# Kernel tuning notes

Hardware: AMD Instinct MI355X
Metric: run time of the kernel (lower is better)

The kernel has to match this reference:

```python
import jax, jax.numpy as jnp
import numpy as np

B, S, D = 8, 512, 512
H, DK = 64, 8          # 64 heads hardcoded in SelfAttentiveLBLBiLM
WIDTH = 16             # local window width
NL = 2                 # highway layers
N = S + 2 * WIDTH      # padded sequence length


def setup_inputs() -> dict:
    key = jax.random.key(0)
    ks = jax.random.split(key, 12)
    s = 0.02
    return {
        "inputs": jax.random.normal(ks[0], (B, S, D), jnp.float32),
        "left_pad": jax.random.normal(ks[1], (WIDTH, D), jnp.float32) * s,
        "right_pad": jax.random.normal(ks[2], (WIDTH, D), jnp.float32) * s,
        "l_Wqkv": jax.random.normal(ks[3], (3, D, D), jnp.float32) * s,
        "l_bqkv": jnp.zeros((3, D), jnp.float32),
        "l_Wo": jax.random.normal(ks[4], (D, D), jnp.float32) * s,
        "l_bo": jnp.zeros((D,), jnp.float32),
        "r_Wqkv": jax.random.normal(ks[5], (3, D, D), jnp.float32) * s,
        "r_bqkv": jnp.zeros((3, D), jnp.float32),
        "r_Wo": jax.random.normal(ks[6], (D, D), jnp.float32) * s,
        "r_bo": jnp.zeros((D,), jnp.float32),
        "lhw_W": jax.random.normal(ks[7], (NL, 2 * D, D), jnp.float32) * s,
        "lhw_b": jnp.zeros((NL, 2 * D), jnp.float32),
        "rhw_W": jax.random.normal(ks[8], (NL, 2 * D, D), jnp.float32) * s,
        "rhw_b": jnp.zeros((NL, 2 * D), jnp.float32),
    }


def _masks(n, width):
    i = jnp.arange(n)[:, None]
    j = jnp.arange(n)[None, :]
    # local_mask: triu(k=-width-1) * (1 - triu(k=1)) -> i-width-1 <= j <= i
    left = (j <= i) & (j >= i - width - 1)
    # right mask is the full flip of the left mask
    right = (j >= i) & (j <= i + width + 1)
    return left, right


def _mha(x, Wqkv, bqkv, Wo, bo, mask):
    b, n, d = x.shape
    # torch Linear: y = x @ W.T + b, W is [out, in]
    qkv = jnp.einsum("bnd,tod->tbno", x, Wqkv) + bqkv[:, None, None, :]
    q, k, v = [t.reshape(b, n, H, DK).transpose(0, 2, 1, 3) for t in qkv]
    scores = jnp.einsum("bhqd,bhkd->bhqk", q, k) / jnp.sqrt(jnp.float32(DK))
    scores = jnp.where(mask[None, None], scores, jnp.float32(-1e9))
    p = jax.nn.softmax(scores, axis=-1)
    out = jnp.einsum("bhqk,bhkd->bhqd", p, v)
    out = out.transpose(0, 2, 1, 3).reshape(b, n, d)
    return out @ Wo.T + bo


def _highway(x, Ws, bs):
    for l in range(NL):
        proj = x @ Ws[l].T + bs[l]
        nonlin = jax.nn.relu(proj[..., :D])
        gate = jax.nn.sigmoid(proj[..., D:])
        x = gate * x + (1.0 - gate) * nonlin
    return x


def reference(inputs, left_pad, right_pad, l_Wqkv, l_bqkv, l_Wo, l_bo,
              r_Wqkv, r_bqkv, r_Wo, r_bo, lhw_W, lhw_b, rhw_W, rhw_b):
    b = inputs.shape[0]
    new_inputs = jnp.concatenate(
        [jnp.broadcast_to(left_pad[None], (b, WIDTH, D)), inputs,
         jnp.broadcast_to(right_pad[None], (b, WIDTH, D))], axis=1)  # [B, N, D]
    left_mask, right_mask = _masks(N, WIDTH)
    new_left = _mha(new_inputs, l_Wqkv, l_bqkv, l_Wo, l_bo, left_mask)
    new_right = _mha(new_inputs, r_Wqkv, r_bqkv, r_Wo, r_bo, right_mask)
    # per-step loop indexes position start + width -> slice [WIDTH : WIDTH + S]
    left_out = _highway(new_left[:, WIDTH:WIDTH + S], lhw_W, lhw_b)
    right_out = _highway(new_right[:, WIDTH:WIDTH + S], rhw_W, rhw_b)
    last = jnp.concatenate([left_out, right_out], axis=-1)  # [B, S, 2D]
    all_layers = last[None]  # [1, B, S, 2D] (single layer stacked on dim 0)
    return (all_layers, last)
```

## Files before the change

### kernel.cpp

```cpp
#include <hip/hip_runtime.h>
#include <math.h>

#define B_ 8
#define S_ 512
#define D_ 512
#define WIDTH_ 16
#define NSEQ 544
#define MROWS 4352
#define MOUT 4096
#define OUTHALF 4194304

typedef _Float16 half8 __attribute__((ext_vector_type(8)));
typedef _Float16 half4 __attribute__((ext_vector_type(4)));
typedef float floatx4 __attribute__((ext_vector_type(4)));

#define GLD16(g, l) __builtin_amdgcn_global_load_lds(                          \
    (const __attribute__((address_space(1))) void*)(g),                        \
    (__attribute__((address_space(3))) void*)(l), 16, 0, 0)

#define WAIT_VM(n)  asm volatile("s_waitcnt vmcnt(" #n ")" ::: "memory")
#define WAIT_LGKM0() asm volatile("s_waitcnt lgkmcnt(0)" ::: "memory")
#define BARRIER()                                                              \
    do {                                                                       \
        __builtin_amdgcn_s_barrier();                                          \
        asm volatile("" ::: "memory");                                         \
    } while (0)

__device__ __forceinline__ float sigmoidf_(float x) {
    return 1.f / (1.f + __expf(-x));
}

__device__ __forceinline__ void xcd_swz(const int nx, const int ny,
                                        int& bx, int& by, int& bz) {
    const int flat = blockIdx.x + nx * (blockIdx.y + ny * blockIdx.z);
    const int nwg  = nx * ny * 2;
    const int t2   = (flat & 7) * (nwg >> 3) + (flat >> 3);
    bz = t2 / (nx * ny);
    const int rem = t2 - bz * nx * ny;
    by = rem / nx;
    bx = rem - by * nx;
}

__global__ __launch_bounds__(256)
void gemm_qkv(const _Float16* __restrict__ A,
              const _Float16* __restrict__ B0, const _Float16* __restrict__ B1,
              const float* __restrict__ bias0, const float* __restrict__ bias1,
              _Float16* __restrict__ C16) {
    const int lda = 512, ldb = 512, ldc = 1536;
    __shared__ _Float16 SH[16384];
    int bx, by, bz;
    xcd_swz(12, 34, bx, by, bz);
    const int t    = threadIdx.x;
    const int wave = t >> 6;
    const int lane = t & 63;
    const int bm = by * 128;
    const int bn = bx * 128;
    const int z  = bz;
    const _Float16* B = z ? B1 : B0;
    const float* bias = z ? bias1 : bias0;
    _Float16* C = C16 + (size_t)z * MROWS * 1536;
    const int wm = (wave & 1) * 64;
    const int wn = (wave >> 1) * 64;

    const int inst = wave * 2;
    const int r0 = inst * 16 + (lane >> 2);
    const int kf = (lane & 3) * 8;

    const _Float16* Ag0 = A + (size_t)(bm + r0) * lda + kf;
    const _Float16* Ag1 = Ag0 + (size_t)16 * lda;
    const _Float16* Bg0 = B + (size_t)(bn + r0) * ldb + kf;
    const _Float16* Bg1 = Bg0 + (size_t)16 * ldb;
    const int so = inst * 512;

    const int fr = lane & 15;
    const int fq = (lane >> 4) * 8;

    floatx4 acc[4][4] = {};

#define QKV_STAGE(bf_, koff_)                                                  \
    do {                                                                       \
        GLD16(Ag0 + (koff_), &SH[(bf_) * 4096 + so]);                          \
        GLD16(Ag1 + (koff_), &SH[(bf_) * 4096 + so + 512]);                    \
        GLD16(Bg0 + (koff_), &SH[8192 + (bf_) * 4096 + so]);                   \
        GLD16(Bg1 + (koff_), &SH[8192 + (bf_) * 4096 + so + 512]);             \
    } while (0)

    QKV_STAGE(0, 0);
    QKV_STAGE(1, 32);

#pragma unroll
    for (int tt = 0; tt < 16; tt++) {
        const int c = tt & 1;
        if (tt == 15) WAIT_VM(0);
        else          WAIT_VM(4);
        BARRIER();
        half8 af[4], bf[4];
#pragma unroll
        for (int s = 0; s < 4; s++) {
            af[s] = *(const half8*)&SH[c * 4096 + (wm + s * 16 + fr) * 32 + fq];
            bf[s] = *(const half8*)&SH[8192 + c * 4096 + (wn + s * 16 + fr) * 32 + fq];
        }
        WAIT_LGKM0();
        BARRIER();
        if (tt + 2 < 16) QKV_STAGE(c, (tt + 2) * 32);
#pragma unroll
        for (int i = 0; i < 4; i++)
#pragma unroll
            for (int j = 0; j < 4; j++)
                acc[i][j] = __builtin_amdgcn_mfma_f32_16x16x32_f16(
                    af[i], bf[j], acc[i][j], 0, 0, 0);
    }
#undef QKV_STAGE

    const int rq = (lane >> 4) * 4;
    const int cc = lane & 15;
#pragma unroll
    for (int i = 0; i < 4; i++) {
#pragma unroll
        for (int j = 0; j < 4; j++) {
            const int col = wn + j * 16 + cc;
            const float bv = bias[bn + col];
#pragma unroll
            for (int r = 0; r < 4; r++)
                SH[(wm + i * 16 + rq + r) * 128 + col] =
                    (_Float16)(acc[i][j][r] + bv);
        }
    }
    WAIT_LGKM0();
    BARRIER();
#pragma unroll
    for (int it = 0; it < 8; it++) {
        const int flat = it * 256 + t;
        const int row = flat >> 4;
        const int ch  = flat & 15;
        *(half8*)&C[(size_t)(bm + row) * ldc + bn + ch * 8] =
            *(const half8*)&SH[row * 128 + ch * 8];
    }
}

__global__ __launch_bounds__(256)
void gemm_wo(const _Float16* __restrict__ Aall,
             const _Float16* __restrict__ B0, const _Float16* __restrict__ B1,
             const float* __restrict__ bias0, const float* __restrict__ bias1,
             _Float16* __restrict__ x16base) {
    const int lda = 512, ldb = 512;
    __shared__ _Float16 As[2][64 * 32];
    __shared__ _Float16 Bs[2][128 * 32];
    int bx, by, bz;
    xcd_swz(4, 68, bx, by, bz);
    const int t    = threadIdx.x;
    const int wave = t >> 6;
    const int lane = t & 63;
    const int bm = by * 64;
    const int bn = bx * 128;
    const int z  = bz;
    const _Float16* A = Aall + (size_t)z * MROWS * 512;
    const _Float16* B = z ? B1 : B0;
    const float* bias = z ? bias1 : bias0;
    _Float16* x16 = x16base + (size_t)z * MOUT * 512;

    const int wm = (wave & 1) * 32;
    const int wn = (wave >> 1) * 64;

    const int rA = wave * 16 + (lane >> 2);
    const int rB = wave * 32 + (lane >> 2);
    const int kf = (lane & 3) * 8;

    const _Float16* Ag0 = A + (size_t)(bm + rA) * lda + kf;
    const _Float16* Bg0 = B + (size_t)(bn + rB) * ldb + kf;
    const _Float16* Bg1 = Bg0 + (size_t)16 * ldb;
    const int soA = wave * 512;
    const int soB = wave * 1024;

    const int fr = lane & 15;
    const int fq = (lane >> 4) * 8;

    floatx4 acc[2][4] = {};

#define WO_STAGE(bf_, koff_)                                                   \
    do {                                                                       \
        GLD16(Ag0 + (koff_), &As[bf_][soA]);                                   \
        GLD16(Bg0 + (koff_), &Bs[bf_][soB]);                                   \
        GLD16(Bg1 + (koff_), &Bs[bf_][soB + 512]);                             \
    } while (0)

    WO_STAGE(0, 0);
    WO_STAGE(1, 32);

#pragma unroll
    for (int tt = 0; tt < 16; tt++) {
        const int c = tt & 1;
        if (tt == 15) WAIT_VM(0);
        else          WAIT_VM(3);
        BARRIER();
        half8 af[2], bf[4];
#pragma unroll
        for (int s = 0; s < 2; s++)
            af[s] = *(const half8*)&As[c][(wm + s * 16 + fr) * 32 + fq];
#pragma unroll
        for (int s = 0; s < 4; s++)
            bf[s] = *(const half8*)&Bs[c][(wn + s * 16 + fr) * 32 + fq];
        WAIT_LGKM0();
        BARRIER();
        if (tt + 2 < 16) WO_STAGE(c, (tt + 2) * 32);
#pragma unroll
        for (int i = 0; i < 2; i++)
#pragma unroll
            for (int j = 0; j < 4; j++)
                acc[i][j] = __builtin_amdgcn_mfma_f32_16x16x32_f16(
                    af[i], bf[j], acc[i][j], 0, 0, 0);
    }
#undef WO_STAGE

    const int rq = (lane >> 4) * 4;
    const int cc = lane & 15;
#pragma unroll
    for (int i = 0; i < 2; i++) {
        const int rbase = bm + wm + i * 16 + rq;
#pragma unroll
        for (int r = 0; r < 4; r++) {
            const int row = rbase + r;
            const int b = row / NSEQ;
            const int s = row - b * NSEQ;
            if (s < WIDTH_ || s >= WIDTH_ + S_) continue;
            const int m = b * S_ + s - WIDTH_;
#pragma unroll
            for (int j = 0; j < 4; j++) {
                const int col = bn + wn + j * 16 + cc;
                x16[(size_t)m * 512 + col] = (_Float16)(acc[i][j][r] + bias[col]);
            }
        }
    }
}

__global__ __launch_bounds__(256)
void gemm_hw(const _Float16* __restrict__ x16inbase,
             const _Float16* __restrict__ W0, const _Float16* __restrict__ W1,
             const float* __restrict__ b0, const float* __restrict__ b1,
             _Float16* __restrict__ x16outbase,
             float* __restrict__ outlastbase,
             float* __restrict__ outallbase) {
    const int lda = 512, ldb = 512;
    __shared__ _Float16 SA[8192];
    __shared__ _Float16 Bn[2][64 * 32];
    __shared__ _Float16 Bg[2][64 * 32];
    int bx, by, bz;
    xcd_swz(8, 32, bx, by, bz);
    const int t    = threadIdx.x;
    const int wave = t >> 6;
    const int lane = t & 63;
    const int bm = by * 128;
    const int bn = bx * 64;
    const int z  = bz;
    const _Float16* A = x16inbase + (size_t)z * MOUT * 512;
    const _Float16* W = z ? W1 : W0;
    const float* bias = z ? b1 : b0;
    _Float16* x16out = x16outbase ? x16outbase + (size_t)z * MOUT * 512 : nullptr;

    const int wm = (wave & 1) * 64;
    const int wn = (wave >> 1) * 32;

    const int rA = wave * 32 + (lane >> 2);
    const int rB = wave * 16 + (lane >> 2);
    const int kf = (lane & 3) * 8;

    const _Float16* Ag0 = A + (size_t)(bm + rA) * lda + kf;
    const _Float16* Ag1 = Ag0 + (size_t)16 * lda;
    const _Float16* Bn0 = W + (size_t)(bn + rB) * ldb + kf;
    const _Float16* Bg0 = W + (size_t)(512 + bn + rB) * ldb + kf;
    const int soA = wave * 1024;
    const int soB = wave * 512;

    const int fr = lane & 15;
    const int fq = (lane >> 4) * 8;

    floatx4 accn[4][2] = {};
    floatx4 accg[4][2] = {};

#define HW_STAGE(bf_, koff_)                                                   \
    do {                                                                       \
        GLD16(Ag0 + (koff_), &SA[(bf_) * 4096 + soA]);                         \
        GLD16(Ag1 + (koff_), &SA[(bf_) * 4096 + soA + 512]);                   \
        GLD16(Bn0 + (koff_), &Bn[bf_][soB]);                                   \
        GLD16(Bg0 + (koff_), &Bg[bf_][soB]);                                   \
    } while (0)

    HW_STAGE(0, 0);
    HW_STAGE(1, 32);

#pragma unroll
    for (int tt = 0; tt < 16; tt++) {
        const int c = tt & 1;
        if (tt == 15) WAIT_VM(0);
        else          WAIT_VM(4);
        BARRIER();
        half8 af[4], bnf[2], bgf[2];
#pragma unroll
        for (int s = 0; s < 4; s++)
            af[s] = *(const half8*)&SA[c * 4096 + (wm + s * 16 + fr) * 32 + fq];
#pragma unroll
        for (int s = 0; s < 2; s++) {
            bnf[s] = *(const half8*)&Bn[c][(wn + s * 16 + fr) * 32 + fq];
            bgf[s] = *(const half8*)&Bg[c][(wn + s * 16 + fr) * 32 + fq];
        }
        WAIT_LGKM0();
        BARRIER();
        if (tt + 2 < 16) HW_STAGE(c, (tt + 2) * 32);
#pragma unroll
        for (int i = 0; i < 4; i++)
#pragma unroll
            for (int j = 0; j < 2; j++) {
                accn[i][j] = __builtin_amdgcn_mfma_f32_16x16x32_f16(
                    af[i], bnf[j], accn[i][j], 0, 0, 0);
                accg[i][j] = __builtin_amdgcn_mfma_f32_16x16x32_f16(
                    af[i], bgf[j], accg[i][j], 0, 0, 0);
            }
    }
#undef HW_STAGE

    const int rq = (lane >> 4) * 4;
    const int cc = lane & 15;
    if (x16out) {
#pragma unroll
        for (int i = 0; i < 4; i++) {
#pragma unroll
            for (int j = 0; j < 2; j++) {
                const int col = wn + j * 16 + cc;
                const float bnl = bias[bn + col];
                const float bgt = bias[512 + bn + col];
#pragma unroll
                for (int r = 0; r < 4; r++) {
                    const int row = wm + i * 16 + rq + r;
                    const float nl = fmaxf(accn[i][j][r] + bnl, 0.f);
                    const float g  = sigmoidf_(accg[i][j][r] + bgt);
                    const float xo = (float)A[(size_t)(bm + row) * 512 + bn + col];
                    SA[row * 64 + col] = (_Float16)(g * xo + (1.f - g) * nl);
                }
            }
        }
        WAIT_LGKM0();
        BARRIER();
#pragma unroll
        for (int it = 0; it < 4; it++) {
            const int flat = it * 256 + t;
            const int row = flat >> 3;
            const int ch  = flat & 7;
            *(half8*)&x16out[(size_t)(bm + row) * 512 + bn + ch * 8] =
                *(const half8*)&SA[row * 64 + ch * 8];
        }
    } else {
        float* outlast = outlastbase + z * 512;
        float* outall  = outallbase  + z * 512;
#pragma unroll
        for (int i = 0; i < 4; i++) {
            const int rbase = bm + wm + i * 16 + rq;
#pragma unroll
            for (int j = 0; j < 2; j++) {
                const int col = bn + wn + j * 16 + cc;
                const float bnl = bias[col];
                const float bgt = bias[512 + col];
#pragma unroll
                for (int r = 0; r < 4; r++) {
                    const int row = rbase + r;
                    const float nl = fmaxf(accn[i][j][r] + bnl, 0.f);
                    const float g  = sigmoidf_(accg[i][j][r] + bgt);
                    const float xo = (float)A[(size_t)row * 512 + col];
                    const float v  = g * xo + (1.f - g) * nl;
                    outlast[(size_t)row * 1024 + col] = v;
                    outall[(size_t)row * 1024 + col] = v;
                }
            }
        }
    }
}

__global__ __launch_bounds__(256)
void attn_win(const _Float16* __restrict__ qkvall, _Float16* __restrict__ attall) {
    const int sb  = (blockIdx.x & 7) * 68 + (blockIdx.x >> 3);
    const int wid = threadIdx.x >> 6;
    const int h   = threadIdx.x & 63;
    const int wflat = sb * 4 + wid;
    const int ig  = wflat % 136;
    const int db  = wflat / 136;
    const int b   = db & 7;
    const int dir = db >> 3;
    const int i0  = ig * 4;
    const int dlo = dir ? 0 : -17;
    const _Float16* qkv = qkvall + (size_t)dir * MROWS * 1536;
    _Float16* att = attall + (size_t)dir * MROWS * 512;
    const size_t rowb = (size_t)b * NSEQ;
    const float scale = 0.35355339059327373f;

    float q[4][8];
#pragma unroll
    for (int tq = 0; tq < 4; tq++) {
        const half8 q8 = *(const half8*)(qkv + (rowb + i0 + tq) * 1536 + h * 8);
#pragma unroll
        for (int d = 0; d < 8; d++) q[tq][d] = (float)q8[d];
    }

    float o[4][8] = {};
    float sum[4] = {};
    const int j0 = i0 + dlo;

#pragma unroll
    for (int jj = 0; jj < 21; jj++) {
        const int j = j0 + jj;
        if (j < 0 || j > NSEQ - 1) continue;
        const size_t jbase = (rowb + j) * 1536 + h * 8;
        const half8 k8 = *(const half8*)(qkv + jbase + 512);
        const half8 v8 = *(const half8*)(qkv + jbase + 1024);
        float kv[8], vv[8];
#pragma unroll
        for (int d = 0; d < 8; d++) { kv[d] = (float)k8[d]; vv[d] = (float)v8[d]; }
#pragma unroll
        for (int tq = 0; tq < 4; tq++) {
            if (jj < tq || jj > tq + 17) continue;
            float d = 0.f;
#pragma unroll
            for (int dd = 0; dd < 8; dd++) d = fmaf(q[tq][dd], kv[dd], d);
            const float p = __expf(d * scale);
            sum[tq] += p;
#pragma unroll
            for (int dd = 0; dd < 8; dd++) o[tq][dd] = fmaf(p, vv[dd], o[tq][dd]);
        }
    }

#pragma unroll
    for (int tq = 0; tq < 4; tq++) {
        const float inv = 1.f / sum[tq];
        half8 o16;
#pragma unroll
        for (int d = 0; d < 8; d++) o16[d] = (_Float16)(o[tq][d] * inv);
        *(half8*)&att[(rowb + i0 + tq) * 512 + h * 8] = o16;
    }
}

__global__ void prep(const float* __restrict__ lq, const float* __restrict__ rq,
                     const float* __restrict__ lo, const float* __restrict__ ro,
                     const float* __restrict__ lh, const float* __restrict__ rh,
                     _Float16* __restrict__ wdst,
                     const float* __restrict__ inp,
                     const float* __restrict__ lp,
                     const float* __restrict__ rp,
                     _Float16* __restrict__ padX) {
    const int gb = blockIdx.x;
    if (gb < 4096) {
        int idx = gb * 256 + threadIdx.x;
        const float* src; int off;
        if      (idx < 196608) { src = lq; off = idx; }
        else if (idx < 393216) { src = rq; off = idx - 196608; }
        else if (idx < 458752) { src = lo; off = idx - 393216; }
        else if (idx < 524288) { src = ro; off = idx - 458752; }
        else if (idx < 786432) { src = lh; off = idx - 524288; }
        else                   { src = rh; off = idx - 786432; }
        const float4 v = ((const float4*)src)[off];
        half4 h = { (_Float16)v.x, (_Float16)v.y, (_Float16)v.z, (_Float16)v.w };
        ((half4*)wdst)[idx] = h;
    } else {
        int idx = (gb - 4096) * 256 + threadIdx.x;
        const int c4 = idx & 127;
        const int t  = idx >> 7;
        const int n = t % NSEQ;
        const int b = t / NSEQ;
        const float* src;
        if (n < WIDTH_)            src = lp + n * 512;
        else if (n < WIDTH_ + S_)  src = inp + ((size_t)(b * S_ + n - WIDTH_)) * 512;
        else                       src = rp + (n - WIDTH_ - S_) * 512;
        const float4 v = *(const float4*)(src + c4 * 4);
        half4 h = { (_Float16)v.x, (_Float16)v.y, (_Float16)v.z, (_Float16)v.w };
        *(half4*)&padX[(size_t)t * 512 + c4 * 4] = h;
    }
}

extern "C" void kernel_launch(void* const* d_in, const int* in_sizes, int n_in,
                              void* d_out, int out_size, void* d_ws, size_t ws_size,
                              hipStream_t stream) {
    const float* inputs    = (const float*)d_in[0];
    const float* left_pad  = (const float*)d_in[1];
    const float* right_pad = (const float*)d_in[2];
    const float* l_Wqkv = (const float*)d_in[3];
    const float* l_bqkv = (const float*)d_in[4];
    const float* l_Wo   = (const float*)d_in[5];
    const float* l_bo   = (const float*)d_in[6];
    const float* r_Wqkv = (const float*)d_in[7];
    const float* r_bqkv = (const float*)d_in[8];
    const float* r_Wo   = (const float*)d_in[9];
    const float* r_bo   = (const float*)d_in[10];
    const float* lhw_W  = (const float*)d_in[11];
    const float* lhw_b  = (const float*)d_in[12];
    const float* rhw_W  = (const float*)d_in[13];
    const float* rhw_b  = (const float*)d_in[14];

    float* out = (float*)d_out;
    _Float16* h = (_Float16*)d_ws;

    _Float16* padX16 = h;
    _Float16* w16    = h + 2228224;
    _Float16* lqkv16 = w16;
    _Float16* rqkv16 = w16 + 786432;
    _Float16* lWo16  = w16 + 1572864;
    _Float16* rWo16  = w16 + 1835008;
    _Float16* lhw16  = w16 + 2097152;
    _Float16* rhw16  = w16 + 3145728;
    _Float16* qkv16  = h + 6422528;
    _Float16* att16  = h + 19791872;
    _Float16* x16a   = h + 24248320;
    _Float16* x16b   = h + 28442624;

    float* out_all  = out;
    float* out_last = out + OUTHALF;

    prep<<<6272, 256, 0, stream>>>(l_Wqkv, r_Wqkv, l_Wo, r_Wo, lhw_W, rhw_W, w16,
                                   inputs, left_pad, right_pad, padX16);

    gemm_qkv<<<dim3(12, 34, 2), 256, 0, stream>>>(
        padX16, lqkv16, rqkv16, l_bqkv, r_bqkv, qkv16);

    attn_win<<<dim3(544), 256, 0, stream>>>(qkv16, att16);

    gemm_wo<<<dim3(4, 68, 2), 256, 0, stream>>>(
        att16, lWo16, rWo16, l_bo, r_bo, x16a);

    gemm_hw<<<dim3(8, 32, 2), 256, 0, stream>>>(
        x16a, lhw16, rhw16, lhw_b, rhw_b, x16b, nullptr, nullptr);
    gemm_hw<<<dim3(8, 32, 2), 256, 0, stream>>>(
        x16b, lhw16 + 524288, rhw16 + 524288, lhw_b + 1024, rhw_b + 1024,
        nullptr, out_last, out_all);
}
```

Baseline: 185.4 us.

## Triple-buffer GEMM K-loops and stage epilogues through LDS for coalesced stores

Moves the three GEMM kernels (qkv, wo, highway) from double to triple LDS buffering. The prefetch for stage tt+2 is now issued right after the first barrier, which removes the second barrier in each K iteration. The wo and highway epilogues now stage results in shared memory and write them back as vectorized, coalesced stores. The highway kernel also bulk-loads its residual input tile into LDS instead of doing scattered global reads. The cost is more LDS per block, which could reduce occupancy, plus extra barriers in the epilogues.

```diff
diff --git a/kernel.cpp b/kernel.cpp
--- a/kernel.cpp
+++ b/kernel.cpp
@@ -19,7 +19,11 @@
     (__attribute__((address_space(3))) void*)(l), 16, 0, 0)
 
 #define WAIT_VM(n)  asm volatile("s_waitcnt vmcnt(" #n ")" ::: "memory")
-#define WAIT_LGKM0() asm volatile("s_waitcnt lgkmcnt(0)" ::: "memory")
+#define WAIT_LGKM0()                                                           \
+    do {                                                                       \
+        asm volatile("s_waitcnt lgkmcnt(0)" ::: "memory");                     \
+        __builtin_amdgcn_sched_barrier(0);                                     \
+    } while (0)
 #define BARRIER()                                                              \
     do {                                                                       \
         __builtin_amdgcn_s_barrier();                                          \
@@ -47,7 +51,7 @@
               const float* __restrict__ bias0, const float* __restrict__ bias1,
               _Float16* __restrict__ C16) {
     const int lda = 512, ldb = 512, ldc = 1536;
-    __shared__ _Float16 SH[16384];
+    __shared__ _Float16 SH[24576];
     int bx, by, bz;
     xcd_swz(12, 34, bx, by, bz);
     const int t    = threadIdx.x;
@@ -81,8 +85,8 @@
     do {                                                                       \
         GLD16(Ag0 + (koff_), &SH[(bf_) * 4096 + so]);                          \
         GLD16(Ag1 + (koff_), &SH[(bf_) * 4096 + so + 512]);                    \
-        GLD16(Bg0 + (koff_), &SH[8192 + (bf_) * 4096 + so]);                   \
-        GLD16(Bg1 + (koff_), &SH[8192 + (bf_) * 4096 + so + 512]);             \
+        GLD16(Bg0 + (koff_), &SH[12288 + (bf_) * 4096 + so]);                  \
+        GLD16(Bg1 + (koff_), &SH[12288 + (bf_) * 4096 + so + 512]);            \
     } while (0)
 
     QKV_STAGE(0, 0);
@@ -90,19 +94,18 @@
 
 #pragma unroll
     for (int tt = 0; tt < 16; tt++) {
-        const int c = tt & 1;
+        const int c = tt % 3;
         if (tt == 15) WAIT_VM(0);
         else          WAIT_VM(4);
         BARRIER();
+        if (tt + 2 < 16) QKV_STAGE((tt + 2) % 3, (tt + 2) * 32);
         half8 af[4], bf[4];
 #pragma unroll
         for (int s = 0; s < 4; s++) {
             af[s] = *(const half8*)&SH[c * 4096 + (wm + s * 16 + fr) * 32 + fq];
-            bf[s] = *(const half8*)&SH[8192 + c * 4096 + (wn + s * 16 + fr) * 32 + fq];
+            bf[s] = *(const half8*)&SH[12288 + c * 4096 + (wn + s * 16 + fr) * 32 + fq];
         }
         WAIT_LGKM0();
-        BARRIER();
-        if (tt + 2 < 16) QKV_STAGE(c, (tt + 2) * 32);
 #pragma unroll
         for (int i = 0; i < 4; i++)
 #pragma unroll
@@ -112,6 +115,7 @@
     }
 #undef QKV_STAGE
 
+    BARRIER();
     const int rq = (lane >> 4) * 4;
     const int cc = lane & 15;
 #pragma unroll
@@ -144,8 +148,7 @@
              const float* __restrict__ bias0, const float* __restrict__ bias1,
              _Float16* __restrict__ x16base) {
     const int lda = 512, ldb = 512;
-    __shared__ _Float16 As[2][64 * 32];
-    __shared__ _Float16 Bs[2][128 * 32];
+    __shared__ _Float16 SH[18432];
     int bx, by, bz;
     xcd_swz(4, 68, bx, by, bz);
     const int t    = threadIdx.x;
@@ -179,9 +182,9 @@
 
 #define WO_STAGE(bf_, koff_)                                                   \
     do {                                                                       \
-        GLD16(Ag0 + (koff_), &As[bf_][soA]);                                   \
-        GLD16(Bg0 + (koff_), &Bs[bf_][soB]);                                   \
-        GLD16(Bg1 + (koff_), &Bs[bf_][soB + 512]);                             \
+        GLD16(Ag0 + (koff_), &SH[(bf_) * 2048 + soA]);                         \
+        GLD16(Bg0 + (koff_), &SH[6144 + (bf_) * 4096 + soB]);                  \
+        GLD16(Bg1 + (koff_), &SH[6144 + (bf_) * 4096 + soB + 512]);            \
     } while (0)
 
     WO_STAGE(0, 0);
@@ -189,20 +192,19 @@
 
 #pragma unroll
     for (int tt = 0; tt < 16; tt++) {
-        const int c = tt & 1;
+        const int c = tt % 3;
         if (tt == 15) WAIT_VM(0);
         else          WAIT_VM(3);
         BARRIER();
+        if (tt + 2 < 16) WO_STAGE((tt + 2) % 3, (tt + 2) * 32);
         half8 af[2], bf[4];
 #pragma unroll
         for (int s = 0; s < 2; s++)
-            af[s] = *(const half8*)&As[c][(wm + s * 16 + fr) * 32 + fq];
+            af[s] = *(const half8*)&SH[c * 2048 + (wm + s * 16 + fr) * 32 + fq];
 #pragma unroll
         for (int s = 0; s < 4; s++)
-            bf[s] = *(const half8*)&Bs[c][(wn + s * 16 + fr) * 32 + fq];
+            bf[s] = *(const half8*)&SH[6144 + c * 4096 + (wn + s * 16 + fr) * 32 + fq];
         WAIT_LGKM0();
-        BARRIER();
-        if (tt + 2 < 16) WO_STAGE(c, (tt + 2) * 32);
 #pragma unroll
         for (int i = 0; i < 2; i++)
 #pragma unroll
@@ -212,23 +214,35 @@
     }
 #undef WO_STAGE
 
+    BARRIER();
     const int rq = (lane >> 4) * 4;
     const int cc = lane & 15;
 #pragma unroll
     for (int i = 0; i < 2; i++) {
-        const int rbase = bm + wm + i * 16 + rq;
-#pragma unroll
-        for (int r = 0; r < 4; r++) {
-            const int row = rbase + r;
-            const int b = row / NSEQ;
-            const int s = row - b * NSEQ;
-            if (s < WIDTH_ || s >= WIDTH_ + S_) continue;
+#pragma unroll
+        for (int j = 0; j < 4; j++) {
+            const int col = wn + j * 16 + cc;
+            const float bv = bias[bn + col];
+#pragma unroll
+            for (int r = 0; r < 4; r++)
+                SH[(wm + i * 16 + rq + r) * 128 + col] =
+                    (_Float16)(acc[i][j][r] + bv);
+        }
+    }
+    WAIT_LGKM0();
+    BARRIER();
+#pragma unroll
+    for (int it = 0; it < 4; it++) {
+        const int flat = it * 256 + t;
+        const int row = flat >> 4;
+        const int ch  = flat & 15;
+        const int grow = bm + row;
+        const int b = grow / NSEQ;
+        const int s = grow - b * NSEQ;
+        if (s >= WIDTH_ && s < WIDTH_ + S_) {
             const int m = b * S_ + s - WIDTH_;
-#pragma unroll
-            for (int j = 0; j < 4; j++) {
-                const int col = bn + wn + j * 16 + cc;
-                x16[(size_t)m * 512 + col] = (_Float16)(acc[i][j][r] + bias[col]);
-            }
+            *(half8*)&x16[(size_t)m * 512 + bn + ch * 8] =
+                *(const half8*)&SH[row * 128 + ch * 8];
         }
     }
 }
@@ -241,9 +255,7 @@
              float* __restrict__ outlastbase,
              float* __restrict__ outallbase) {
     const int lda = 512, ldb = 512;
-    __shared__ _Float16 SA[8192];
-    __shared__ _Float16 Bn[2][64 * 32];
-    __shared__ _Float16 Bg[2][64 * 32];
+    __shared__ _Float16 SH[24576];
     int bx, by, bz;
     xcd_swz(8, 32, bx, by, bz);
     const int t    = threadIdx.x;
@@ -279,10 +291,10 @@
 
 #define HW_STAGE(bf_, koff_)                                                   \
     do {                                                                       \
-        GLD16(Ag0 + (koff_), &SA[(bf_) * 4096 + soA]);                         \
-        GLD16(Ag1 + (koff_), &SA[(bf_) * 4096 + soA + 512]);                   \
-        GLD16(Bn0 + (koff_), &Bn[bf_][soB]);                                   \
-        GLD16(Bg0 + (koff_), &Bg[bf_][soB]);                                   \
+        GLD16(Ag0 + (koff_), &SH[(bf_) * 4096 + soA]);                         \
+        GLD16(Ag1 + (koff_), &SH[(bf_) * 4096 + soA + 512]);                   \
+        GLD16(Bn0 + (koff_), &SH[12288 + (bf_) * 2048 + soB]);                 \
+        GLD16(Bg0 + (koff_), &SH[18432 + (bf_) * 2048 + soB]);                 \
     } while (0)
 
     HW_STAGE(0, 0);
@@ -290,22 +302,21 @@
 
 #pragma unroll
     for (int tt = 0; tt < 16; tt++) {
-        const int c = tt & 1;
+        const int c = tt % 3;
         if (tt == 15) WAIT_VM(0);
         else          WAIT_VM(4);
         BARRIER();
+        if (tt + 2 < 16) HW_STAGE((tt + 2) % 3, (tt + 2) * 32);
         half8 af[4], bnf[2], bgf[2];
 #pragma unroll
         for (int s = 0; s < 4; s++)
-            af[s] = *(const half8*)&SA[c * 4096 + (wm + s * 16 + fr) * 32 + fq];
+            af[s] = *(const half8*)&SH[c * 4096 + (wm + s * 16 + fr) * 32 + fq];
 #pragma unroll
         for (int s = 0; s < 2; s++) {
-            bnf[s] = *(const half8*)&Bn[c][(wn + s * 16 + fr) * 32 + fq];
-            bgf[s] = *(const half8*)&Bg[c][(wn + s * 16 + fr) * 32 + fq];
+            bnf[s] = *(const half8*)&SH[12288 + c * 2048 + (wn + s * 16 + fr) * 32 + fq];
+            bgf[s] = *(const half8*)&SH[18432 + c * 2048 + (wn + s * 16 + fr) * 32 + fq];
         }
         WAIT_LGKM0();
-        BARRIER();
-        if (tt + 2 < 16) HW_STAGE(c, (tt + 2) * 32);
 #pragma unroll
         for (int i = 0; i < 4; i++)
 #pragma unroll
@@ -318,6 +329,19 @@
     }
 #undef HW_STAGE
 
+    BARRIER();
+    {
+        const int e0 = wave * 4;
+#pragma unroll
+        for (int ii = 0; ii < 4; ii++) {
+            const int einst = e0 + ii;
+            GLD16(A + (size_t)(bm + einst * 8 + (lane >> 3)) * 512 + bn + (lane & 7) * 8,
+                  &SH[einst * 512]);
+        }
+    }
+    WAIT_VM(0);
+    BARRIER();
+
     const int rq = (lane >> 4) * 4;
     const int cc = lane & 15;
     if (x16out) {
@@ -333,8 +357,8 @@
                     const int row = wm + i * 16 + rq + r;
                     const float nl = fmaxf(accn[i][j][r] + bnl, 0.f);
                     const float g  = sigmoidf_(accg[i][j][r] + bgt);
-                    const float xo = (float)A[(size_t)(bm + row) * 512 + bn + col];
-                    SA[row * 64 + col] = (_Float16)(g * xo + (1.f - g) * nl);
+                    const float xo = (float)SH[row * 64 + col];
+                    SH[8192 + row * 64 + col] = (_Float16)(g * xo + (1.f - g) * nl);
                 }
             }
         }
@@ -346,30 +370,46 @@
             const int row = flat >> 3;
             const int ch  = flat & 7;
             *(half8*)&x16out[(size_t)(bm + row) * 512 + bn + ch * 8] =
-                *(const half8*)&SA[row * 64 + ch * 8];
+                *(const half8*)&SH[8192 + row * 64 + ch * 8];
         }
     } else {
+        float* SF = (float*)&SH[8192];
         float* outlast = outlastbase + z * 512;
         float* outall  = outallbase  + z * 512;
 #pragma unroll
-        for (int i = 0; i < 4; i++) {
-            const int rbase = bm + wm + i * 16 + rq;
-#pragma unroll
-            for (int j = 0; j < 2; j++) {
-                const int col = bn + wn + j * 16 + cc;
-                const float bnl = bias[col];
-                const float bgt = bias[512 + col];
-#pragma unroll
-                for (int r = 0; r < 4; r++) {
-                    const int row = rbase + r;
-                    const float nl = fmaxf(accn[i][j][r] + bnl, 0.f);
-                    const float g  = sigmoidf_(accg[i][j][r] + bgt);
-                    const float xo = (float)A[(size_t)row * 512 + col];
-                    const float v  = g * xo + (1.f - g) * nl;
-                    outlast[(size_t)row * 1024 + col] = v;
-                    outall[(size_t)row * 1024 + col] = v;
+        for (int hh = 0; hh < 2; hh++) {
+            if ((wave & 1) == hh) {
+#pragma unroll
+                for (int i = 0; i < 4; i++) {
+#pragma unroll
+                    for (int j = 0; j < 2; j++) {
+                        const int col = wn + j * 16 + cc;
+                        const float bnl = bias[bn + col];
+                        const float bgt = bias[512 + bn + col];
+#pragma unroll
+                        for (int r = 0; r < 4; r++) {
+                            const int row = wm + i * 16 + rq + r;
+                            const float nl = fmaxf(accn[i][j][r] + bnl, 0.f);
+                            const float g  = sigmoidf_(accg[i][j][r] + bgt);
+                            const float xo = (float)SH[row * 64 + col];
+                            SF[(row - 64 * hh) * 64 + col] = g * xo + (1.f - g) * nl;
+                        }
+                    }
                 }
             }
+            WAIT_LGKM0();
+            BARRIER();
+#pragma unroll
+            for (int it = 0; it < 4; it++) {
+                const int flat = it * 256 + t;
+                const int row = flat >> 4;
+                const int c4  = flat & 15;
+                const float4 vv = *(const float4*)&SF[row * 64 + c4 * 4];
+                const size_t gro = (size_t)(bm + 64 * hh + row) * 1024 + bn + c4 * 4;
+                *(float4*)&outlast[gro] = vv;
+                *(float4*)&outall[gro]  = vv;
+            }
+            BARRIER();
         }
     }
 }
```

Result: slower. 192.6 us (+3.9%).

## Widen highway GEMM tile to 128 columns with 512 threads; 8 queries per attention wave

Applied to the files above, without the earlier changes.

The highway GEMM now uses 512-thread blocks that compute a 128x128 output tile (in both nonlin and gate) over half as many blocks. Shared memory is unified into one buffer and each wave issues three async loads per stage. The windowed attention kernel now has each wave process 8 consecutive query rows instead of 4, so each K/V row load is reused across more queries. This cuts redundant global reads, at the cost of more registers per thread and fewer blocks in flight.

```diff
diff --git a/kernel.cpp b/kernel.cpp
--- a/kernel.cpp
+++ b/kernel.cpp
@@ -233,24 +233,21 @@
     }
 }
 
-__global__ __launch_bounds__(256)
+__global__ __launch_bounds__(512)
 void gemm_hw(const _Float16* __restrict__ x16inbase,
              const _Float16* __restrict__ W0, const _Float16* __restrict__ W1,
              const float* __restrict__ b0, const float* __restrict__ b1,
              _Float16* __restrict__ x16outbase,
              float* __restrict__ outlastbase,
              float* __restrict__ outallbase) {
-    const int lda = 512, ldb = 512;
-    __shared__ _Float16 SA[8192];
-    __shared__ _Float16 Bn[2][64 * 32];
-    __shared__ _Float16 Bg[2][64 * 32];
+    __shared__ _Float16 SH[24576];
     int bx, by, bz;
-    xcd_swz(8, 32, bx, by, bz);
+    xcd_swz(4, 32, bx, by, bz);
     const int t    = threadIdx.x;
     const int wave = t >> 6;
     const int lane = t & 63;
     const int bm = by * 128;
-    const int bn = bx * 64;
+    const int bn = bx * 128;
     const int z  = bz;
     const _Float16* A = x16inbase + (size_t)z * MOUT * 512;
     const _Float16* W = z ? W1 : W0;
@@ -260,16 +257,13 @@
     const int wm = (wave & 1) * 64;
     const int wn = (wave >> 1) * 32;
 
-    const int rA = wave * 32 + (lane >> 2);
-    const int rB = wave * 16 + (lane >> 2);
+    const int rS = wave * 16 + (lane >> 2);
     const int kf = (lane & 3) * 8;
 
-    const _Float16* Ag0 = A + (size_t)(bm + rA) * lda + kf;
-    const _Float16* Ag1 = Ag0 + (size_t)16 * lda;
-    const _Float16* Bn0 = W + (size_t)(bn + rB) * ldb + kf;
-    const _Float16* Bg0 = W + (size_t)(512 + bn + rB) * ldb + kf;
-    const int soA = wave * 1024;
-    const int soB = wave * 512;
+    const _Float16* Ag0 = A + (size_t)(bm + rS) * 512 + kf;
+    const _Float16* Bn0 = W + (size_t)(bn + rS) * 512 + kf;
+    const _Float16* Bg0 = W + (size_t)(512 + bn + rS) * 512 + kf;
+    const int so = wave * 512;
 
     const int fr = lane & 15;
     const int fq = (lane >> 4) * 8;
@@ -279,10 +273,9 @@
 
 #define HW_STAGE(bf_, koff_)                                                   \
     do {                                                                       \
-        GLD16(Ag0 + (koff_), &SA[(bf_) * 4096 + soA]);                         \
-        GLD16(Ag1 + (koff_), &SA[(bf_) * 4096 + soA + 512]);                   \
-        GLD16(Bn0 + (koff_), &Bn[bf_][soB]);                                   \
-        GLD16(Bg0 + (koff_), &Bg[bf_][soB]);                                   \
+        GLD16(Ag0 + (koff_), &SH[(bf_) * 4096 + so]);                          \
+        GLD16(Bn0 + (koff_), &SH[8192 + (bf_) * 4096 + so]);                   \
+        GLD16(Bg0 + (koff_), &SH[16384 + (bf_) * 4096 + so]);                  \
     } while (0)
 
     HW_STAGE(0, 0);
@@ -292,16 +285,16 @@
     for (int tt = 0; tt < 16; tt++) {
         const int c = tt & 1;
         if (tt == 15) WAIT_VM(0);
-        else          WAIT_VM(4);
+        else          WAIT_VM(3);
         BARRIER();
         half8 af[4], bnf[2], bgf[2];
 #pragma unroll
         for (int s = 0; s < 4; s++)
-            af[s] = *(const half8*)&SA[c * 4096 + (wm + s * 16 + fr) * 32 + fq];
+            af[s] = *(const half8*)&SH[c * 4096 + (wm + s * 16 + fr) * 32 + fq];
 #pragma unroll
         for (int s = 0; s < 2; s++) {
-            bnf[s] = *(const half8*)&Bn[c][(wn + s * 16 + fr) * 32 + fq];
-            bgf[s] = *(const half8*)&Bg[c][(wn + s * 16 + fr) * 32 + fq];
+            bnf[s] = *(const half8*)&SH[8192 + c * 4096 + (wn + s * 16 + fr) * 32 + fq];
+            bgf[s] = *(const half8*)&SH[16384 + c * 4096 + (wn + s * 16 + fr) * 32 + fq];
         }
         WAIT_LGKM0();
         BARRIER();
@@ -334,7 +327,7 @@
                     const float nl = fmaxf(accn[i][j][r] + bnl, 0.f);
                     const float g  = sigmoidf_(accg[i][j][r] + bgt);
                     const float xo = (float)A[(size_t)(bm + row) * 512 + bn + col];
-                    SA[row * 64 + col] = (_Float16)(g * xo + (1.f - g) * nl);
+                    SH[row * 128 + col] = (_Float16)(g * xo + (1.f - g) * nl);
                 }
             }
         }
@@ -342,11 +335,11 @@
         BARRIER();
 #pragma unroll
         for (int it = 0; it < 4; it++) {
-            const int flat = it * 256 + t;
-            const int row = flat >> 3;
-            const int ch  = flat & 7;
+            const int flat = it * 512 + t;
+            const int row = flat >> 4;
+            const int ch  = flat & 15;
             *(half8*)&x16out[(size_t)(bm + row) * 512 + bn + ch * 8] =
-                *(const half8*)&SA[row * 64 + ch * 8];
+                *(const half8*)&SH[row * 128 + ch * 8];
         }
     } else {
         float* outlast = outlastbase + z * 512;
@@ -364,7 +357,7 @@
                     const int row = rbase + r;
                     const float nl = fmaxf(accn[i][j][r] + bnl, 0.f);
                     const float g  = sigmoidf_(accg[i][j][r] + bgt);
-                    const float xo = (float)A[(size_t)row * 512 + col];
+                    const float xo = (float)A[(size_t)row * 512 + col - bn + bn];
                     const float v  = g * xo + (1.f - g) * nl;
                     outlast[(size_t)row * 1024 + col] = v;
                     outall[(size_t)row * 1024 + col] = v;
@@ -376,35 +369,35 @@
 
 __global__ __launch_bounds__(256)
 void attn_win(const _Float16* __restrict__ qkvall, _Float16* __restrict__ attall) {
-    const int sb  = (blockIdx.x & 7) * 68 + (blockIdx.x >> 3);
+    const int sb  = (blockIdx.x & 7) * 34 + (blockIdx.x >> 3);
     const int wid = threadIdx.x >> 6;
     const int h   = threadIdx.x & 63;
     const int wflat = sb * 4 + wid;
-    const int ig  = wflat % 136;
-    const int db  = wflat / 136;
+    const int ig  = wflat % 68;
+    const int db  = wflat / 68;
     const int b   = db & 7;
     const int dir = db >> 3;
-    const int i0  = ig * 4;
+    const int i0  = ig * 8;
     const int dlo = dir ? 0 : -17;
     const _Float16* qkv = qkvall + (size_t)dir * MROWS * 1536;
     _Float16* att = attall + (size_t)dir * MROWS * 512;
     const size_t rowb = (size_t)b * NSEQ;
     const float scale = 0.35355339059327373f;
 
-    float q[4][8];
-#pragma unroll
-    for (int tq = 0; tq < 4; tq++) {
+    float q[8][8];
+#pragma unroll
+    for (int tq = 0; tq < 8; tq++) {
         const half8 q8 = *(const half8*)(qkv + (rowb + i0 + tq) * 1536 + h * 8);
 #pragma unroll
         for (int d = 0; d < 8; d++) q[tq][d] = (float)q8[d];
     }
 
-    float o[4][8] = {};
-    float sum[4] = {};
+    float o[8][8] = {};
+    float sum[8] = {};
     const int j0 = i0 + dlo;
 
 #pragma unroll
-    for (int jj = 0; jj < 21; jj++) {
+    for (int jj = 0; jj < 25; jj++) {
         const int j = j0 + jj;
         if (j < 0 || j > NSEQ - 1) continue;
         const size_t jbase = (rowb + j) * 1536 + h * 8;
@@ -414,7 +407,7 @@
 #pragma unroll
         for (int d = 0; d < 8; d++) { kv[d] = (float)k8[d]; vv[d] = (float)v8[d]; }
 #pragma unroll
-        for (int tq = 0; tq < 4; tq++) {
+        for (int tq = 0; tq < 8; tq++) {
             if (jj < tq || jj > tq + 17) continue;
             float d = 0.f;
 #pragma unroll
@@ -427,7 +420,7 @@
     }
 
 #pragma unroll
-    for (int tq = 0; tq < 4; tq++) {
+    for (int tq = 0; tq < 8; tq++) {
         const float inv = 1.f / sum[tq];
         half8 o16;
 #pragma unroll
@@ -517,14 +510,14 @@
     gemm_qkv<<<dim3(12, 34, 2), 256, 0, stream>>>(
         padX16, lqkv16, rqkv16, l_bqkv, r_bqkv, qkv16);
 
-    attn_win<<<dim3(544), 256, 0, stream>>>(qkv16, att16);
+    attn_win<<<dim3(272), 256, 0, stream>>>(qkv16, att16);
 
     gemm_wo<<<dim3(4, 68, 2), 256, 0, stream>>>(
         att16, lWo16, rWo16, l_bo, r_bo, x16a);
 
-    gemm_hw<<<dim3(8, 32, 2), 256, 0, stream>>>(
+    gemm_hw<<<dim3(4, 32, 2), 512, 0, stream>>>(
         x16a, lhw16, rhw16, lhw_b, rhw_b, x16b, nullptr, nullptr);
-    gemm_hw<<<dim3(8, 32, 2), 256, 0, stream>>>(
+    gemm_hw<<<dim3(4, 32, 2), 512, 0, stream>>>(
         x16b, lhw16 + 524288, rhw16 + 524288, lhw_b + 1024, rhw_b + 1024,
         nullptr, out_last, out_all);
 }
```

Measured after the change: 188.8 us. Within noise of the previous version (+1.8%).
